# Performance work log

Hardware: AMD Instinct MI355X
Metric: run time of the kernel (lower is better)

The kernel has to match this reference:

```python
import jax, jax.numpy as jnp
import numpy as np

B, IN_SIZE, OUT_SIZE = 4096, 256, 64


def _mask(in_size, out_size):
    # True everywhere EXCEPT each feature's own diagonal block (matches torch buffer).
    col_block = jnp.arange(in_size * out_size) // out_size          # [in*out]
    return col_block[None, :] != jnp.arange(in_size)[:, None]       # [in, in*out] bool


def setup_inputs() -> dict:
    key = jax.random.key(0)
    k1, k2, k3 = jax.random.split(key, 3)
    x = jax.random.normal(k1, (B, IN_SIZE), dtype=jnp.float32)
    weights = jax.random.normal(k2, (IN_SIZE, IN_SIZE * OUT_SIZE), dtype=jnp.float32)
    bias = jax.random.uniform(k3, (IN_SIZE * OUT_SIZE,), dtype=jnp.float32)
    return {"x": x, "weights": weights, "bias": bias}


def reference(x, weights, bias):
    in_size, io = weights.shape
    out_size = io // in_size
    mask = _mask(in_size, out_size).astype(weights.dtype)
    # out = x @ (weights * mask) + bias ; mask zeroes each feature's own block,
    # so output block i depends on all inputs except x_i.
    out = x @ (weights * mask) + bias                                # [B, in*out]
    return out.reshape(-1, in_size, out_size)                        # [B, in, out]
```

## Files before the change

kernel.cpp:

```cpp
#include <hip/hip_runtime.h>
#include <hip/hip_bf16.h>

#define M_DIM 4096
#define N_DIM 16384
#define K_DIM 256

typedef short short8 __attribute__((ext_vector_type(8)));
typedef float f32x4 __attribute__((ext_vector_type(4)));
typedef unsigned int u32x4 __attribute__((ext_vector_type(4)));

__device__ __forceinline__ unsigned int pk2bf(float lo, float hi) {
    unsigned int a = __float_as_uint(lo);
    unsigned int b = __float_as_uint(hi);
    a = (a + 0x7FFFu + ((a >> 16) & 1u)) >> 16;
    b = (b + 0x7FFFu + ((b >> 16) & 1u)) & 0xFFFF0000u;
    return a | b;
}

__global__ __launch_bounds__(256) void convert_kernel(const float* __restrict__ W,
                                                      const float* __restrict__ x,
                                                      unsigned short* __restrict__ Wt,
                                                      unsigned short* __restrict__ xb) {
    const int bx = blockIdx.x;
    const int t  = threadIdx.x;
    if (bx < 512) {
        __shared__ unsigned short tile[128][64];
        const int n0  = (bx & 127) * 128;
        const int kc0 = (bx >> 7) * 64;
        const int nn  = t & 127;
        const int kh  = (t >> 7) * 32;
        const int jm  = (n0 + nn) >> 6;
        const int sw  = (nn & 7) << 3;
        #pragma unroll
        for (int kk = 0; kk < 32; kk += 8) {
            float v[8];
            #pragma unroll
            for (int j = 0; j < 8; ++j) {
                const int k = kc0 + kh + kk + j;
                const float f = W[(size_t)k * N_DIM + n0 + nn];
                v[j] = (k == jm) ? 0.0f : f;
            }
            u32x4 p = { pk2bf(v[0], v[1]), pk2bf(v[2], v[3]),
                        pk2bf(v[4], v[5]), pk2bf(v[6], v[7]) };
            *(u32x4*)&tile[nn][(kh + kk) ^ sw] = p;
        }
        __syncthreads();
        const int kc = (t & 7) * 8;
        const int nr = t >> 3;
        #pragma unroll
        for (int it = 0; it < 4; ++it) {
            const int n = it * 32 + nr;
            u32x4 p = *(const u32x4*)&tile[n][kc ^ ((n & 7) << 3)];
            *(u32x4*)(Wt + (size_t)(n0 + n) * K_DIM + kc0 + kc) = p;
        }
    } else {
        const size_t base = ((size_t)(bx - 512) * 256 + t) * 8;
        float4 a = *(const float4*)(x + base);
        float4 b = *(const float4*)(x + base + 4);
        u32x4 p = { pk2bf(a.x, a.y), pk2bf(a.z, a.w),
                    pk2bf(b.x, b.y), pk2bf(b.z, b.w) };
        *(u32x4*)(xb + base) = p;
    }
}

constexpr int BM = 128, BN = 128, BK = 64;

__global__ __launch_bounds__(256, 2) void gemm_kernel(
        const unsigned short* __restrict__ Abf,
        const unsigned short* __restrict__ Bbf,
        const float* __restrict__ bias,
        float* __restrict__ out) {
    __shared__ __align__(16) unsigned char smem[65536];
    auto As = (unsigned short (*)[BM][BK])(smem);
    auto Bs = (unsigned short (*)[BN][BK])(smem + 32768);
    float* Cs = (float*)smem;

    const int bid = blockIdx.x;
    const int xcd = bid & 7;
    const int q   = bid >> 3;
    const int n0  = (xcd * 16 + (q & 15)) * BN;
    const int m0  = (q >> 4) * BM;

    const int t    = threadIdx.x;
    const int lane = t & 63;
    const int wave = t >> 6;
    const int wm   = (wave >> 1) * 64;
    const int wn   = (wave & 1) * 64;
    const int lr   = lane & 15;
    const int lk   = (lane >> 4) * 8;

    const int srow = t >> 3;
    const int selk = (t & 7) * 8;

    const unsigned short* gA = Abf + (size_t)(m0 + srow) * K_DIM + selk;
    const unsigned short* gB = Bbf + (size_t)(n0 + srow) * K_DIM + selk;

    u32x4 ra[4], rb[4];

    auto ldreg = [&](int kt) {
        #pragma unroll
        for (int r = 0; r < 4; ++r) {
            ra[r] = *(const u32x4*)(gA + (size_t)(r * 32) * K_DIM + kt * BK);
            rb[r] = *(const u32x4*)(gB + (size_t)(r * 32) * K_DIM + kt * BK);
        }
    };
    auto dswrite = [&](int buf) {
        #pragma unroll
        for (int r = 0; r < 4; ++r) {
            const int row = srow + r * 32;
            const int c   = selk ^ ((row & 7) << 3);
            *(u32x4*)&As[buf][row][c] = ra[r];
            *(u32x4*)&Bs[buf][row][c] = rb[r];
        }
    };

    f32x4 acc[4][4] = {};

    ldreg(0);
    dswrite(0);
    __syncthreads();

    #pragma unroll
    for (int kt = 0; kt < 4; ++kt) {
        const int buf = kt & 1;
        if (kt < 3) ldreg(kt + 1);
        #pragma unroll
        for (int ks = 0; ks < 2; ++ks) {
            short8 af[4], bfr[4];
            #pragma unroll
            for (int mi = 0; mi < 4; ++mi) {
                const int row = wm + mi * 16 + lr;
                const int c   = (ks * 32 + lk) ^ ((row & 7) << 3);
                af[mi] = *(const short8*)&As[buf][row][c];
            }
            #pragma unroll
            for (int ni = 0; ni < 4; ++ni) {
                const int row = wn + ni * 16 + lr;
                const int c   = (ks * 32 + lk) ^ ((row & 7) << 3);
                bfr[ni] = *(const short8*)&Bs[buf][row][c];
            }
            #pragma unroll
            for (int mi = 0; mi < 4; ++mi)
                #pragma unroll
                for (int ni = 0; ni < 4; ++ni)
                    acc[mi][ni] = __builtin_amdgcn_mfma_f32_16x16x32_bf16(
                        bfr[ni], af[mi], acc[mi][ni], 0, 0, 0);
        }
        if (kt < 3) {
            dswrite(buf ^ 1);
            __syncthreads();
        }
    }

    __syncthreads();

    {
        const int rl0 = wm + lr;
        const int nl0 = wn + (lane >> 4) * 4;
        #pragma unroll
        for (int mi = 0; mi < 4; ++mi) {
            const int rl = rl0 + mi * 16;
            const int sx = (rl & 7) << 2;
            #pragma unroll
            for (int ni = 0; ni < 4; ++ni) {
                const int nl = (nl0 + ni * 16) ^ sx;
                *(f32x4*)&Cs[rl * BN + nl] = acc[mi][ni];
            }
        }
    }
    __syncthreads();

    {
        const int col4 = (t & 31) * 4;
        const float4 bv = *(const float4*)(bias + n0 + col4);
        #pragma unroll
        for (int p = 0; p < 16; ++p) {
            const int row = p * 8 + (t >> 5);
            const int cs  = col4 ^ ((row & 7) << 2);
            f32x4 v = *(const f32x4*)&Cs[row * BN + cs];
            v[0] += bv.x; v[1] += bv.y; v[2] += bv.z; v[3] += bv.w;
            *(f32x4*)(out + (size_t)(m0 + row) * N_DIM + n0 + col4) = v;
        }
    }
}

__global__ __launch_bounds__(256) void fallback_kernel(const float* __restrict__ x,
                                                       const float* __restrict__ W,
                                                       const float* __restrict__ bias,
                                                       float* __restrict__ out) {
    const size_t gid = (size_t)blockIdx.x * 256 + threadIdx.x;
    const size_t row = gid / (N_DIM / 8);
    const int    c0  = (int)(gid % (N_DIM / 8)) * 8;
    const int    jm  = c0 >> 6;
    float acc[8] = {0, 0, 0, 0, 0, 0, 0, 0};
    const float* xr = x + row * K_DIM;
    for (int k = 0; k < K_DIM; ++k) {
        const float xv = (k == jm) ? 0.0f : xr[k];
        const float4* wr = (const float4*)(W + (size_t)k * N_DIM + c0);
        float4 w0 = wr[0], w1 = wr[1];
        acc[0] += xv * w0.x; acc[1] += xv * w0.y;
        acc[2] += xv * w0.z; acc[3] += xv * w0.w;
        acc[4] += xv * w1.x; acc[5] += xv * w1.y;
        acc[6] += xv * w1.z; acc[7] += xv * w1.w;
    }
    float* o = out + row * N_DIM + c0;
    #pragma unroll
    for (int j = 0; j < 8; ++j) o[j] = acc[j] + bias[c0 + j];
}

extern "C" void kernel_launch(void* const* d_in, const int* in_sizes, int n_in,
                              void* d_out, int out_size, void* d_ws, size_t ws_size,
                              hipStream_t stream) {
    const float* x    = (const float*)d_in[0];
    const float* W    = (const float*)d_in[1];
    const float* bias = (const float*)d_in[2];
    float* out        = (float*)d_out;

    const size_t wt_bytes = (size_t)N_DIM * K_DIM * 2;
    const size_t xb_bytes = (size_t)M_DIM * K_DIM * 2;

    if (ws_size >= wt_bytes + xb_bytes) {
        unsigned short* Wt = (unsigned short*)d_ws;
        unsigned short* xb = (unsigned short*)((char*)d_ws + wt_bytes);

        convert_kernel<<<512 + (M_DIM * K_DIM / 8) / 256, 256, 0, stream>>>(W, x, Wt, xb);
        gemm_kernel<<<(M_DIM / BM) * (N_DIM / BN), 256, 0, stream>>>(xb, Wt, bias, out);
    } else {
        const size_t total = (size_t)M_DIM * N_DIM / 8;
        fallback_kernel<<<(unsigned)(total / 256), 256, 0, stream>>>(x, W, bias, out);
    }
}
```

Measured before the change: 78.95 us.

## Pre-swizzle x into MFMA fragment layout and load A directly to registers

The conversion kernel now writes bf16 x in a fragment-major layout matching the MFMA A-operand lane order. The GEMM then loads A fragments straight from global memory into registers, double-buffered across k-tiles, and stages only B through LDS. This removes the A-side LDS writes and reads and halves LDS traffic per block. In exchange each wave issues its own global loads for A with no sharing between the two waves that use the same rows, and register pressure rises from the extra A buffers.

After: 76.02 us. 1.04x faster.

```diff
diff --git a/kernel.cpp b/kernel.cpp
--- a/kernel.cpp
+++ b/kernel.cpp
@@ -54,12 +54,16 @@
             *(u32x4*)(Wt + (size_t)(n0 + n) * K_DIM + kc0 + kc) = p;
         }
     } else {
-        const size_t base = ((size_t)(bx - 512) * 256 + t) * 8;
-        float4 a = *(const float4*)(x + base);
-        float4 b = *(const float4*)(x + base + 4);
+        const int g  = (bx - 512) * 256 + t;
+        const int m  = g >> 5;
+        const int k0 = (g & 31) * 8;
+        const float4 a = *(const float4*)(x + (size_t)m * K_DIM + k0);
+        const float4 b = *(const float4*)(x + (size_t)m * K_DIM + k0 + 4);
         u32x4 p = { pk2bf(a.x, a.y), pk2bf(a.z, a.w),
                     pk2bf(b.x, b.y), pk2bf(b.z, b.w) };
-        *(u32x4*)(xb + base) = p;
+        const int chunk = (m >> 4) * 8 + (k0 >> 5);
+        const int lane  = ((k0 & 31) >> 3) * 16 + (m & 15);
+        ((u32x4*)xb)[chunk * 64 + lane] = p;
     }
 }
 
@@ -71,8 +75,7 @@
         const float* __restrict__ bias,
         float* __restrict__ out) {
     __shared__ __align__(16) unsigned char smem[65536];
-    auto As = (unsigned short (*)[BM][BK])(smem);
-    auto Bs = (unsigned short (*)[BN][BK])(smem + 32768);
+    auto Bs = (unsigned short (*)[BN][BK])(smem);
     float* Cs = (float*)smem;
 
     const int bid = blockIdx.x;
@@ -92,47 +95,52 @@
     const int srow = t >> 3;
     const int selk = (t & 7) * 8;
 
-    const unsigned short* gA = Abf + (size_t)(m0 + srow) * K_DIM + selk;
+    const int mTB = (m0 + wm) >> 4;
+    const short8* gAt = (const short8*)Abf;
+
     const unsigned short* gB = Bbf + (size_t)(n0 + srow) * K_DIM + selk;
 
-    u32x4 ra[4], rb[4];
-
-    auto ldreg = [&](int kt) {
-        #pragma unroll
-        for (int r = 0; r < 4; ++r) {
-            ra[r] = *(const u32x4*)(gA + (size_t)(r * 32) * K_DIM + kt * BK);
+    u32x4 rb[4];
+    auto ldregB = [&](int kt) {
+        #pragma unroll
+        for (int r = 0; r < 4; ++r)
             rb[r] = *(const u32x4*)(gB + (size_t)(r * 32) * K_DIM + kt * BK);
-        }
     };
-    auto dswrite = [&](int buf) {
+    auto dswriteB = [&](int buf) {
         #pragma unroll
         for (int r = 0; r < 4; ++r) {
             const int row = srow + r * 32;
             const int c   = selk ^ ((row & 7) << 3);
-            *(u32x4*)&As[buf][row][c] = ra[r];
             *(u32x4*)&Bs[buf][row][c] = rb[r];
         }
     };
 
+    short8 afc[2][4], afn[2][4];
+    auto ldA = [&](short8 (&dst)[2][4], int kt) {
+        #pragma unroll
+        for (int ks = 0; ks < 2; ++ks)
+            #pragma unroll
+            for (int mi = 0; mi < 4; ++mi)
+                dst[ks][mi] = gAt[(size_t)((mTB + mi) * 8 + kt * 2 + ks) * 64 + lane];
+    };
+
     f32x4 acc[4][4] = {};
 
-    ldreg(0);
-    dswrite(0);
+    ldA(afc, 0);
+    ldregB(0);
+    dswriteB(0);
     __syncthreads();
 
     #pragma unroll
     for (int kt = 0; kt < 4; ++kt) {
         const int buf = kt & 1;
-        if (kt < 3) ldreg(kt + 1);
+        if (kt < 3) {
+            ldA(afn, kt + 1);
+            ldregB(kt + 1);
+        }
         #pragma unroll
         for (int ks = 0; ks < 2; ++ks) {
-            short8 af[4], bfr[4];
-            #pragma unroll
-            for (int mi = 0; mi < 4; ++mi) {
-                const int row = wm + mi * 16 + lr;
-                const int c   = (ks * 32 + lk) ^ ((row & 7) << 3);
-                af[mi] = *(const short8*)&As[buf][row][c];
-            }
+            short8 bfr[4];
             #pragma unroll
             for (int ni = 0; ni < 4; ++ni) {
                 const int row = wn + ni * 16 + lr;
@@ -144,11 +152,16 @@
                 #pragma unroll
                 for (int ni = 0; ni < 4; ++ni)
                     acc[mi][ni] = __builtin_amdgcn_mfma_f32_16x16x32_bf16(
-                        bfr[ni], af[mi], acc[mi][ni], 0, 0, 0);
+                        bfr[ni], afc[ks][mi], acc[mi][ni], 0, 0, 0);
         }
         if (kt < 3) {
-            dswrite(buf ^ 1);
+            dswriteB(buf ^ 1);
             __syncthreads();
+            #pragma unroll
+            for (int ks = 0; ks < 2; ++ks)
+                #pragma unroll
+                for (int mi = 0; mi < 4; ++mi)
+                    afc[ks][mi] = afn[ks][mi];
         }
     }
 
```
